# Optimization experiments

Hardware: AMD Instinct MI355X
Metric: run time of the kernel (lower is better)

The kernel has to match this reference:

```python
import jax, jax.numpy as jnp
import numpy as np

F = 128   # flattened observation features
H = 64    # MLP/LSTM hidden size (hardcoded in module)
A = 15    # number of discrete actions
T = 128   # rollout length (timesteps)
B = 2048  # number of parallel envs (batch)


def setup_inputs() -> dict:
    key = jax.random.key(0)
    ks = jax.random.split(key, 12)
    n = lambda k, sh, s=1.0: jax.random.normal(k, sh, jnp.float32) * s
    return {
        "x": n(ks[0], (T * B, F)),
        "done": (jax.random.uniform(ks[1], (T * B,)) < 0.05).astype(jnp.float32),
        "h0": n(ks[2], (1, B, H)),
        "c0": n(ks[3], (1, B, H)),
        # MLP encoder params (Linear stores y = x @ W + b here, W: [in, out])
        "W1": n(ks[4], (F, H), 0.1), "b1": jnp.zeros((H,), jnp.float32),
        "W2": n(ks[5], (H, H), 0.1), "b2": jnp.zeros((H,), jnp.float32),
        # LSTM params, PyTorch layout: weight_ih [4H, H_in], gate order i,f,g,o
        "Wih": n(ks[6], (4 * H, H), 0.1), "bih": jnp.zeros((4 * H,), jnp.float32),
        "Whh": n(ks[7], (4 * H, H), 0.1), "bhh": jnp.zeros((4 * H,), jnp.float32),
        # actor / critic heads
        "Wa": n(ks[8], (H, A), 0.01), "ba": jnp.zeros((A,), jnp.float32),
        "Wc": n(ks[9], (H, 1), 1.0), "bc": jnp.zeros((1,), jnp.float32),
    }


def reference(x, done, h0, c0, W1, b1, W2, b2, Wih, bih, Whh, bhh, Wa, ba, Wc, bc):
    Bsz, Hh = h0.shape[1], h0.shape[2]
    # MLP encoder: Linear -> Tanh -> Linear -> Tanh
    y = jnp.tanh(x @ W1 + b1)
    y = jnp.tanh(y @ W2 + b2)                 # [T*B, H]
    y = y.reshape(-1, Bsz, Hh)                # [T, B, H]
    d = done.reshape(-1, Bsz)                 # [T, B]

    def step(carry, td):
        h, c = carry
        yt, dt = td
        m = (1.0 - dt)[:, None]               # done-mask hidden reset
        h = h * m
        c = c * m
        g = yt @ Wih.T + bih + h @ Whh.T + bhh  # [B, 4H]
        i, f, gg, o = jnp.split(g, 4, axis=-1)
        c = jax.nn.sigmoid(f) * c + jax.nn.sigmoid(i) * jnp.tanh(gg)
        h = jax.nn.sigmoid(o) * jnp.tanh(c)
        return (h, c), h

    (hT, cT), outs = jax.lax.scan(step, (h0[0], c0[0]), (y, d))
    z = outs.reshape(-1, Hh)                  # [T*B, H]
    logits = z @ Wa + ba                      # Categorical logits
    vf = z @ Wc + bc
    return logits, vf, hT[None], cT[None]
```

## Files before the change

### kernel.cpp

```cpp
#include <hip/hip_runtime.h>
#include <hip/hip_bf16.h>
#include <stdint.h>

typedef __bf16  bf16x8 __attribute__((ext_vector_type(8)));
typedef short   s16x8  __attribute__((ext_vector_type(8)));
typedef int     i32x4  __attribute__((ext_vector_type(4)));
typedef float   f32x4  __attribute__((ext_vector_type(4)));

union Frag { s16x8 s; bf16x8 b; i32x4 i; };

static __device__ __forceinline__ short f2bf(float f) {
    union { float f; unsigned u; } v; v.f = f;
    unsigned r = (v.u + 0x7FFFu + ((v.u >> 16) & 1u)) >> 16;
    return (short)r;
}
static __device__ __forceinline__ float bf2f(short s) {
    union { unsigned u; float f; } v; v.u = ((unsigned)(unsigned short)s) << 16;
    return v.f;
}
static __device__ __forceinline__ float fast_rcp(float x) { return __builtin_amdgcn_rcpf(x); }
static __device__ __forceinline__ float sigm(float x) { return fast_rcp(1.0f + __expf(-x)); }
static __device__ __forceinline__ float tanh_fast(float x) {
    float e = __expf(-2.0f * x);
    return (1.0f - e) * fast_rcp(1.0f + e);
}
static __device__ __forceinline__ f32x4 mfma16(bf16x8 a, bf16x8 b, f32x4 c) {
    return __builtin_amdgcn_mfma_f32_16x16x32_bf16(a, b, c, 0, 0, 0);
}

#define TT 128
#define BB 2048
#define HH 64
#define FF 128
#define AA 15
#define NROWS (TT*BB)
#define NTILES (NROWS/16)
#define LOGITS_OFF 0
#define VF_OFF   3932160
#define HT_OFF   4194304
#define CT_OFF   4325376


__global__ __launch_bounds__(256) void enc_kernel(
    const float* __restrict__ x, const float* __restrict__ W1, const float* __restrict__ b1,
    const float* __restrict__ W2, const float* __restrict__ b2, short* __restrict__ y_sw)
{
    __shared__ short w1t[64][136];
    __shared__ short w2t[64][72];
    __shared__ short c1buf[4][16][72];
    __shared__ short ybuf[4][16][72];

    const int tid  = threadIdx.x;
    const int lane = tid & 63;
    const int w    = tid >> 6;
    const int c    = lane & 15;
    const int q    = lane >> 4;

    for (int i = tid; i < 128*64; i += 256) { int k = i >> 6, n = i & 63; w1t[n][k] = f2bf(W1[i]); }
    for (int i = tid; i < 64*64;  i += 256) { int k = i >> 6, n = i & 63; w2t[n][k] = f2bf(W2[i]); }

    float b1v[4], b2v[4];
#pragma unroll
    for (int ct = 0; ct < 4; ++ct) { b1v[ct] = b1[16*ct + c]; b2v[ct] = b2[16*ct + c]; }
    __syncthreads();

    for (int it = 0; it < 4; ++it) {
        const int wt = it*4096 + blockIdx.x*4 + w;
        const int r0 = wt * 16;
        Frag af[4];
#pragma unroll
        for (int kf = 0; kf < 4; ++kf) {
            const float* xp = x + (size_t)(r0 + c)*FF + 32*kf + 8*q;
            f32x4 x0 = *(const f32x4*)xp;
            f32x4 x1 = *(const f32x4*)(xp + 4);
#pragma unroll
            for (int jj = 0; jj < 4; ++jj) { af[kf].s[jj] = f2bf(x0[jj]); af[kf].s[4+jj] = f2bf(x1[jj]); }
        }
        f32x4 acc[4];
#pragma unroll
        for (int ct = 0; ct < 4; ++ct) acc[ct] = (f32x4){b1v[ct], b1v[ct], b1v[ct], b1v[ct]};
#pragma unroll
        for (int kf = 0; kf < 4; ++kf)
#pragma unroll
            for (int ct = 0; ct < 4; ++ct) {
                Frag bf; bf.s = *(const s16x8*)&w1t[16*ct + c][32*kf + 8*q];
                acc[ct] = mfma16(af[kf].b, bf.b, acc[ct]);
            }
#pragma unroll
        for (int ct = 0; ct < 4; ++ct)
#pragma unroll
            for (int i = 0; i < 4; ++i)
                c1buf[w][4*q + i][16*ct + c] = f2bf(tanh_fast(acc[ct][i]));
        Frag a2[2];
#pragma unroll
        for (int kf = 0; kf < 2; ++kf) a2[kf].s = *(const s16x8*)&c1buf[w][c][32*kf + 8*q];
        f32x4 acc2[4];
#pragma unroll
        for (int ct = 0; ct < 4; ++ct) acc2[ct] = (f32x4){b2v[ct], b2v[ct], b2v[ct], b2v[ct]};
#pragma unroll
        for (int kf = 0; kf < 2; ++kf)
#pragma unroll
            for (int ct = 0; ct < 4; ++ct) {
                Frag bf; bf.s = *(const s16x8*)&w2t[16*ct + c][32*kf + 8*q];
                acc2[ct] = mfma16(a2[kf].b, bf.b, acc2[ct]);
            }
#pragma unroll
        for (int ct = 0; ct < 4; ++ct)
#pragma unroll
            for (int i = 0; i < 4; ++i)
                ybuf[w][4*q + i][16*ct + c] = f2bf(tanh_fast(acc2[ct][i]));
#pragma unroll
        for (int kf = 0; kf < 2; ++kf) {
            s16x8 yv = *(const s16x8*)&ybuf[w][c][32*kf + 8*q];
            *(s16x8*)(y_sw + (size_t)wt*1024 + kf*512 + lane*8) = yv;
        }
    }
}

__global__ __launch_bounds__(256, 1) void scan_kernel(
    const short* __restrict__ y_sw, const float* __restrict__ done,
    const float* __restrict__ h0, const float* __restrict__ c0,
    const float* __restrict__ Wih, const float* __restrict__ bih,
    const float* __restrict__ Whh, const float* __restrict__ bhh,
    short* __restrict__ z_sw, float* __restrict__ hT_out, float* __restrict__ cT_out)
{
    __shared__ short hbuf[2][16][72];

    const int tid  = threadIdx.x;
    const int lane = tid & 63;
    const int w    = tid >> 6;
    const int c    = lane & 15;
    const int q    = lane >> 4;
    const int blk  = blockIdx.x;
    const int b0   = blk * 16;
    const int jcol = 16*w + c;

    Frag  wf[4][4];
    float biasv[4];
#pragma unroll
    for (int a = 0; a < 4; ++a) {
        const int col = 64*a + jcol;
        biasv[a] = bih[col] + bhh[col];
#pragma unroll
        for (int kf = 0; kf < 4; ++kf) {
            const float* wp = (kf < 2) ? (Wih + (size_t)col*HH + 32*kf + 8*q)
                                       : (Whh + (size_t)col*HH + 32*(kf-2) + 8*q);
            f32x4 w0 = *(const f32x4*)wp;
            f32x4 w1 = *(const f32x4*)(wp + 4);
#pragma unroll
            for (int jj = 0; jj < 4; ++jj) { wf[a][kf].s[jj] = f2bf(w0[jj]); wf[a][kf].s[4+jj] = f2bf(w1[jj]); }
        }
    }
    float cst[4];
#pragma unroll
    for (int i = 0; i < 4; ++i) cst[i] = c0[(size_t)(b0 + 4*q + i)*HH + jcol];
    {
        int mm = tid & 15, j4 = tid >> 4;
        f32x4 hv = *(const f32x4*)(h0 + (size_t)(b0 + mm)*HH + 4*j4);
#pragma unroll
        for (int ii = 0; ii < 4; ++ii) hbuf[0][mm][4*j4 + ii] = f2bf(hv[ii]);
    }
    Frag yc0, yc1;
    yc0.s = *(const s16x8*)(y_sw + (size_t)blk*1024 + lane*8);
    yc1.s = *(const s16x8*)(y_sw + (size_t)blk*1024 + 512 + lane*8);
    float dmv = done[b0 + c];
    f32x4 dcv = *(const f32x4*)(done + b0 + 4*q);
    __syncthreads();

    for (int t = 0; t < TT; ++t) {
        const int cur = t & 1, nxt = cur ^ 1;
        Frag hf0, hf1;
        hf0.s = *(const s16x8*)&hbuf[cur][c][8*q];
        hf1.s = *(const s16x8*)&hbuf[cur][c][32 + 8*q];
        if (t > 0) {
            short* zp = z_sw + ((size_t)(t-1)*128 + blk)*1024 + lane*8;
            *(s16x8*)zp         = hf0.s;
            *(s16x8*)(zp + 512) = hf1.s;
        }
        const int msk = (dmv != 0.0f) ? 0 : -1;
        Frag h0m, h1m;
#pragma unroll
        for (int k = 0; k < 4; ++k) { h0m.i[k] = hf0.i[k] & msk; h1m.i[k] = hf1.i[k] & msk; }
        const int tn = (t < TT-1) ? t + 1 : TT-1;
        Frag yn0, yn1;
        yn0.s = *(const s16x8*)(y_sw + ((size_t)tn*128 + blk)*1024 + lane*8);
        yn1.s = *(const s16x8*)(y_sw + ((size_t)tn*128 + blk)*1024 + 512 + lane*8);
        float dmn = done[tn*BB + b0 + c];
        f32x4 dcn = *(const f32x4*)(done + tn*BB + b0 + 4*q);
        f32x4 acc[4];
#pragma unroll
        for (int a = 0; a < 4; ++a) {
            acc[a] = (f32x4){biasv[a], biasv[a], biasv[a], biasv[a]};
            acc[a] = mfma16(yc0.b, wf[a][0].b, acc[a]);
            acc[a] = mfma16(yc1.b, wf[a][1].b, acc[a]);
            acc[a] = mfma16(h0m.b, wf[a][2].b, acc[a]);
            acc[a] = mfma16(h1m.b, wf[a][3].b, acc[a]);
        }
#pragma unroll
        for (int i = 0; i < 4; ++i) {
            float gi = acc[0][i], gf = acc[1][i], gg = acc[2][i], go = acc[3][i];
            float cm = (dcv[i] != 0.0f) ? 0.0f : cst[i];
            float cn = sigm(gf)*cm + sigm(gi)*tanh_fast(gg);
            cst[i] = cn;
            hbuf[nxt][4*q + i][jcol] = f2bf(sigm(go)*tanh_fast(cn));
        }
        yc0 = yn0; yc1 = yn1; dmv = dmn; dcv = dcn;
        __syncthreads();
    }
    {
        Frag hf0, hf1;
        hf0.s = *(const s16x8*)&hbuf[0][c][8*q];
        hf1.s = *(const s16x8*)&hbuf[0][c][32 + 8*q];
        short* zp = z_sw + ((size_t)(TT-1)*128 + blk)*1024 + lane*8;
        *(s16x8*)zp         = hf0.s;
        *(s16x8*)(zp + 512) = hf1.s;
    }
    {
        int mm = tid & 15, j4 = tid >> 4;
        f32x4 hv;
#pragma unroll
        for (int ii = 0; ii < 4; ++ii) hv[ii] = bf2f(hbuf[0][mm][4*j4 + ii]);
        *(f32x4*)(hT_out + (size_t)(b0 + mm)*HH + 4*j4) = hv;
    }
#pragma unroll
    for (int i = 0; i < 4; ++i) cT_out[(size_t)(b0 + 4*q + i)*HH + jcol] = cst[i];
}

__global__ __launch_bounds__(256) void heads_kernel(
    const short* __restrict__ z_sw, const float* __restrict__ Wa, const float* __restrict__ ba,
    const float* __restrict__ Wc, const float* __restrict__ bc, float* __restrict__ out)
{
    const int tid  = threadIdx.x;
    const int lane = tid & 63;
    const int w    = tid >> 6;
    const int n    = lane & 15;
    const int q    = lane >> 4;

    Frag wf[2];
#pragma unroll
    for (int kf = 0; kf < 2; ++kf)
#pragma unroll
        for (int jj = 0; jj < 8; ++jj) {
            int k = 32*kf + 8*q + jj;
            float v = (n < 15) ? Wa[k*AA + n] : Wc[k];
            wf[kf].s[jj] = f2bf(v);
        }
    const float bv = (n < 15) ? ba[n] : bc[0];

    for (int s = 0; s < 16; ++s) {
        const int wt = s*1024 + blockIdx.x*4 + w;
        Frag a0, a1;
        a0.s = *(const s16x8*)(z_sw + (size_t)wt*1024 + lane*8);
        a1.s = *(const s16x8*)(z_sw + (size_t)wt*1024 + 512 + lane*8);
        f32x4 acc = (f32x4){bv, bv, bv, bv};
        acc = mfma16(a0.b, wf[0].b, acc);
        acc = mfma16(a1.b, wf[1].b, acc);
        const int r0 = wt*16 + 4*q;
#pragma unroll
        for (int i = 0; i < 4; ++i) {
            const int row = r0 + i;
            if (n < 15) out[LOGITS_OFF + (size_t)row*AA + n] = acc[i];
            else        out[VF_OFF + row] = acc[i];
        }
    }
}

extern "C" void kernel_launch(void* const* d_in, const int* in_sizes, int n_in,
                              void* d_out, int out_size, void* d_ws, size_t ws_size,
                              hipStream_t stream) {
    const float* x    = (const float*)d_in[0];
    const float* done = (const float*)d_in[1];
    const float* h0   = (const float*)d_in[2];
    const float* c0   = (const float*)d_in[3];
    const float* W1   = (const float*)d_in[4];
    const float* b1   = (const float*)d_in[5];
    const float* W2   = (const float*)d_in[6];
    const float* b2   = (const float*)d_in[7];
    const float* Wih  = (const float*)d_in[8];
    const float* bih  = (const float*)d_in[9];
    const float* Whh  = (const float*)d_in[10];
    const float* bhh  = (const float*)d_in[11];
    const float* Wa   = (const float*)d_in[12];
    const float* ba   = (const float*)d_in[13];
    const float* Wc   = (const float*)d_in[14];
    const float* bc   = (const float*)d_in[15];
    float* out = (float*)d_out;

    short* ws   = (short*)d_ws;
    short* y_sw = ws;
    short* z_sw = ws + 16777216;

    enc_kernel<<<1024, 256, 0, stream>>>(x, W1, b1, W2, b2, y_sw);
    scan_kernel<<<128, 256, 0, stream>>>(y_sw, done, h0, c0, Wih, bih, Whh, bhh,
                                         z_sw, out + HT_OFF, out + CT_OFF);
    heads_kernel<<<256, 256, 0, stream>>>(z_sw, Wa, ba, Wc, bc, out);
}
```

Measured before the change: 331.2 us.

## Fuse actor/critic heads into LSTM scan and stage inputs via async LDS loads

```diff
diff --git a/kernel.cpp b/kernel.cpp
--- a/kernel.cpp
+++ b/kernel.cpp
@@ -28,13 +28,16 @@
     return __builtin_amdgcn_mfma_f32_16x16x32_bf16(a, b, c, 0, 0, 0);
 }
 
+#define GLDS(gp, lp) __builtin_amdgcn_global_load_lds( \
+    (const __attribute__((address_space(1))) void*)(gp), \
+    (__attribute__((address_space(3))) void*)(lp), 16, 0, 0)
+
 #define TT 128
 #define BB 2048
 #define HH 64
 #define FF 128
 #define AA 15
-#define NROWS (TT*BB)
-#define NTILES (NROWS/16)
+#define CH 32
 #define LOGITS_OFF 0
 #define VF_OFF   3932160
 #define HT_OFF   4194304
@@ -122,9 +125,15 @@
     const float* __restrict__ h0, const float* __restrict__ c0,
     const float* __restrict__ Wih, const float* __restrict__ bih,
     const float* __restrict__ Whh, const float* __restrict__ bhh,
-    short* __restrict__ z_sw, float* __restrict__ hT_out, float* __restrict__ cT_out)
+    const float* __restrict__ Wa, const float* __restrict__ ba,
+    const float* __restrict__ Wc, const float* __restrict__ bc,
+    float* __restrict__ out_logits, float* __restrict__ out_vf,
+    float* __restrict__ hT_out, float* __restrict__ cT_out)
 {
+    __shared__ short ybuf[CH][1024];
+    __shared__ float obuf[CH][16][16];
     __shared__ short hbuf[2][16][72];
+    __shared__ float dbuf[TT][16];
 
     const int tid  = threadIdx.x;
     const int lane = tid & 63;
@@ -151,6 +160,16 @@
             for (int jj = 0; jj < 4; ++jj) { wf[a][kf].s[jj] = f2bf(w0[jj]); wf[a][kf].s[4+jj] = f2bf(w1[jj]); }
         }
     }
+    Frag hwf[2]; float hbv;
+#pragma unroll
+    for (int kf = 0; kf < 2; ++kf)
+#pragma unroll
+        for (int jj = 0; jj < 8; ++jj) {
+            int k = 32*kf + 8*q + jj;
+            hwf[kf].s[jj] = f2bf((c < 15) ? Wa[k*AA + c] : Wc[k]);
+        }
+    hbv = (c < 15) ? ba[c] : bc[0];
+
     float cst[4];
 #pragma unroll
     for (int i = 0; i < 4; ++i) cst[i] = c0[(size_t)(b0 + 4*q + i)*HH + jcol];
@@ -160,33 +179,63 @@
 #pragma unroll
         for (int ii = 0; ii < 4; ++ii) hbuf[0][mm][4*j4 + ii] = f2bf(hv[ii]);
     }
-    Frag yc0, yc1;
-    yc0.s = *(const s16x8*)(y_sw + (size_t)blk*1024 + lane*8);
-    yc1.s = *(const s16x8*)(y_sw + (size_t)blk*1024 + 512 + lane*8);
-    float dmv = done[b0 + c];
-    f32x4 dcv = *(const f32x4*)(done + b0 + 4*q);
+#pragma unroll
+    for (int i = 0; i < 2; ++i) {
+        int j = w*2 + i;
+        const float* gp = done + (size_t)(16*j + (lane >> 2))*BB + b0 + 4*(lane & 3);
+        GLDS(gp, &dbuf[16*j][0]);
+    }
+#pragma unroll
+    for (int i = 0; i < 16; ++i) {
+        int idx = w*16 + i, ss = idx >> 1, hh = idx & 1;
+        const short* gp = y_sw + ((size_t)ss*128 + blk)*1024 + hh*512 + lane*8;
+        GLDS(gp, &ybuf[ss][hh*512]);
+    }
+    __builtin_amdgcn_s_waitcnt(0x0F70);
     __syncthreads();
 
     for (int t = 0; t < TT; ++t) {
-        const int cur = t & 1, nxt = cur ^ 1;
+        const int cur = t & 1, nxt = cur ^ 1, s = t & (CH-1);
         Frag hf0, hf1;
         hf0.s = *(const s16x8*)&hbuf[cur][c][8*q];
         hf1.s = *(const s16x8*)&hbuf[cur][c][32 + 8*q];
-        if (t > 0) {
-            short* zp = z_sw + ((size_t)(t-1)*128 + blk)*1024 + lane*8;
-            *(s16x8*)zp         = hf0.s;
-            *(s16x8*)(zp + 512) = hf1.s;
-        }
+        if (t > 0 && ((t-1) & 3) == w) {
+            f32x4 ha = (f32x4){hbv, hbv, hbv, hbv};
+            ha = mfma16(hf0.b, hwf[0].b, ha);
+            ha = mfma16(hf1.b, hwf[1].b, ha);
+            const int slot = (t-1) & (CH-1);
+#pragma unroll
+            for (int i = 0; i < 4; ++i) obuf[slot][4*q + i][c] = ha[i];
+        }
+        if (s == 0 && t > 0) {
+            __syncthreads();
+#pragma unroll
+            for (int i = 0; i < 16; ++i) {
+                int idx = w*16 + i, ss = idx >> 1, hh = idx & 1;
+                const short* gp = y_sw + ((size_t)(t + ss)*128 + blk)*1024 + hh*512 + lane*8;
+                GLDS(gp, &ybuf[ss][hh*512]);
+            }
+#pragma unroll
+            for (int rep = 0; rep < 2; ++rep) {
+                int idx = rep*256 + tid, ss = idx >> 4, rr = idx & 15;
+                size_t row = (size_t)(t - CH + ss)*BB + b0 + rr;
+                const float* ob = &obuf[ss][rr][0];
+                float* lp = out_logits + row*AA;
+#pragma unroll
+                for (int n = 0; n < 15; ++n) lp[n] = ob[n];
+                out_vf[row] = ob[15];
+            }
+            __builtin_amdgcn_s_waitcnt(0x0F70);
+            __syncthreads();
+        }
+        const float dmv = dbuf[t][c];
         const int msk = (dmv != 0.0f) ? 0 : -1;
         Frag h0m, h1m;
 #pragma unroll
         for (int k = 0; k < 4; ++k) { h0m.i[k] = hf0.i[k] & msk; h1m.i[k] = hf1.i[k] & msk; }
-        const int tn = (t < TT-1) ? t + 1 : TT-1;
-        Frag yn0, yn1;
-        yn0.s = *(const s16x8*)(y_sw + ((size_t)tn*128 + blk)*1024 + lane*8);
-        yn1.s = *(const s16x8*)(y_sw + ((size_t)tn*128 + blk)*1024 + 512 + lane*8);
-        float dmn = done[tn*BB + b0 + c];
-        f32x4 dcn = *(const f32x4*)(done + tn*BB + b0 + 4*q);
+        Frag yc0, yc1;
+        yc0.s = *(const s16x8*)&ybuf[s][lane*8];
+        yc1.s = *(const s16x8*)&ybuf[s][512 + lane*8];
         f32x4 acc[4];
 #pragma unroll
         for (int a = 0; a < 4; ++a) {
@@ -196,6 +245,7 @@
             acc[a] = mfma16(h0m.b, wf[a][2].b, acc[a]);
             acc[a] = mfma16(h1m.b, wf[a][3].b, acc[a]);
         }
+        const f32x4 dcv = *(const f32x4*)&dbuf[t][4*q];
 #pragma unroll
         for (int i = 0; i < 4; ++i) {
             float gi = acc[0][i], gf = acc[1][i], gg = acc[2][i], go = acc[3][i];
@@ -204,64 +254,39 @@
             cst[i] = cn;
             hbuf[nxt][4*q + i][jcol] = f2bf(sigm(go)*tanh_fast(cn));
         }
-        yc0 = yn0; yc1 = yn1; dmv = dmn; dcv = dcn;
         __syncthreads();
     }
     {
         Frag hf0, hf1;
         hf0.s = *(const s16x8*)&hbuf[0][c][8*q];
         hf1.s = *(const s16x8*)&hbuf[0][c][32 + 8*q];
-        short* zp = z_sw + ((size_t)(TT-1)*128 + blk)*1024 + lane*8;
-        *(s16x8*)zp         = hf0.s;
-        *(s16x8*)(zp + 512) = hf1.s;
-    }
-    {
-        int mm = tid & 15, j4 = tid >> 4;
-        f32x4 hv;
-#pragma unroll
-        for (int ii = 0; ii < 4; ++ii) hv[ii] = bf2f(hbuf[0][mm][4*j4 + ii]);
-        *(f32x4*)(hT_out + (size_t)(b0 + mm)*HH + 4*j4) = hv;
-    }
-#pragma unroll
-    for (int i = 0; i < 4; ++i) cT_out[(size_t)(b0 + 4*q + i)*HH + jcol] = cst[i];
-}
-
-__global__ __launch_bounds__(256) void heads_kernel(
-    const short* __restrict__ z_sw, const float* __restrict__ Wa, const float* __restrict__ ba,
-    const float* __restrict__ Wc, const float* __restrict__ bc, float* __restrict__ out)
-{
-    const int tid  = threadIdx.x;
-    const int lane = tid & 63;
-    const int w    = tid >> 6;
-    const int n    = lane & 15;
-    const int q    = lane >> 4;
-
-    Frag wf[2];
-#pragma unroll
-    for (int kf = 0; kf < 2; ++kf)
-#pragma unroll
-        for (int jj = 0; jj < 8; ++jj) {
-            int k = 32*kf + 8*q + jj;
-            float v = (n < 15) ? Wa[k*AA + n] : Wc[k];
-            wf[kf].s[jj] = f2bf(v);
-        }
-    const float bv = (n < 15) ? ba[n] : bc[0];
-
-    for (int s = 0; s < 16; ++s) {
-        const int wt = s*1024 + blockIdx.x*4 + w;
-        Frag a0, a1;
-        a0.s = *(const s16x8*)(z_sw + (size_t)wt*1024 + lane*8);
-        a1.s = *(const s16x8*)(z_sw + (size_t)wt*1024 + 512 + lane*8);
-        f32x4 acc = (f32x4){bv, bv, bv, bv};
-        acc = mfma16(a0.b, wf[0].b, acc);
-        acc = mfma16(a1.b, wf[1].b, acc);
-        const int r0 = wt*16 + 4*q;
-#pragma unroll
-        for (int i = 0; i < 4; ++i) {
-            const int row = r0 + i;
-            if (n < 15) out[LOGITS_OFF + (size_t)row*AA + n] = acc[i];
-            else        out[VF_OFF + row] = acc[i];
-        }
+        if (((TT-1) & 3) == w) {
+            f32x4 ha = (f32x4){hbv, hbv, hbv, hbv};
+            ha = mfma16(hf0.b, hwf[0].b, ha);
+            ha = mfma16(hf1.b, hwf[1].b, ha);
+#pragma unroll
+            for (int i = 0; i < 4; ++i) obuf[(TT-1) & (CH-1)][4*q + i][c] = ha[i];
+        }
+        __syncthreads();
+#pragma unroll
+        for (int rep = 0; rep < 2; ++rep) {
+            int idx = rep*256 + tid, ss = idx >> 4, rr = idx & 15;
+            size_t row = (size_t)(TT - CH + ss)*BB + b0 + rr;
+            const float* ob = &obuf[ss][rr][0];
+            float* lp = out_logits + row*AA;
+#pragma unroll
+            for (int n = 0; n < 15; ++n) lp[n] = ob[n];
+            out_vf[row] = ob[15];
+        }
+        {
+            int mm = tid & 15, j4 = tid >> 4;
+            f32x4 hv;
+#pragma unroll
+            for (int ii = 0; ii < 4; ++ii) hv[ii] = bf2f(hbuf[0][mm][4*j4 + ii]);
+            *(f32x4*)(hT_out + (size_t)(b0 + mm)*HH + 4*j4) = hv;
+        }
+#pragma unroll
+        for (int i = 0; i < 4; ++i) cT_out[(size_t)(b0 + 4*q + i)*HH + jcol] = cst[i];
     }
 }
 
@@ -286,12 +311,11 @@
     const float* bc   = (const float*)d_in[15];
     float* out = (float*)d_out;
 
-    short* ws   = (short*)d_ws;
-    short* y_sw = ws;
-    short* z_sw = ws + 16777216;
+    short* y_sw = (short*)d_ws;
 
     enc_kernel<<<1024, 256, 0, stream>>>(x, W1, b1, W2, b2, y_sw);
     scan_kernel<<<128, 256, 0, stream>>>(y_sw, done, h0, c0, Wih, bih, Whh, bhh,
-                                         z_sw, out + HT_OFF, out + CT_OFF);
-    heads_kernel<<<256, 256, 0, stream>>>(z_sw, Wa, ba, Wc, bc, out);
-}
+                                         Wa, ba, Wc, bc,
+                                         out + LOGITS_OFF, out + VF_OFF,
+                                         out + HT_OFF, out + CT_OFF);
+}
```

Result: no change. 330.7 us (-0.1%).
